# Kernel tuning notes

Measured on AMD Instinct MI355X. Metric: run time of the kernel, lower is better.

Reference implementation:

```python
import jax, jax.numpy as jnp
import numpy as np

B, H, C, PX, PY = 2, 16, 4, 16, 16
EXTRA = 64
HD = 64
N = C * PX * PY + EXTRA


def setup_inputs() -> dict:
    key = jax.random.key(0)
    ks = jax.random.split(key, 8)
    q = jax.random.normal(ks[0], (B, H, N, HD), jnp.float32)
    k = jax.random.normal(ks[1], (B, H, N, HD), jnp.float32)
    v = jax.random.normal(ks[2], (B, H, N, HD), jnp.float32)
    # valid SE(3) world-to-camera matrices: rotation via QR (det fixed to +1)
    A = jax.random.normal(ks[3], (B, C, 3, 3), jnp.float32)
    Q, _ = jnp.linalg.qr(A)
    det = jnp.linalg.det(Q)
    Q = Q * det[..., None, None]
    t = 0.5 * jax.random.normal(ks[4], (B, C, 3), jnp.float32)
    top = jnp.concatenate([Q, t[..., None]], -1)
    bot = jnp.broadcast_to(jnp.array([0.0, 0.0, 0.0, 1.0], jnp.float32), (B, C, 1, 4))
    viewmats = jnp.concatenate([top, bot], -2)
    # pinhole intrinsics (no skew)
    fx = 300.0 + 10.0 * jax.random.uniform(ks[5], (B, C))
    fy = 300.0 + 10.0 * jax.random.uniform(ks[6], (B, C))
    z = jnp.zeros((B, C)); o = jnp.ones((B, C))
    cx = 128.0 * o; cy = 128.0 * o
    Ks = jnp.stack([jnp.stack([fx, z, cx], -1), jnp.stack([z, fy, cy], -1), jnp.stack([z, z, o], -1)], -2)
    spatial_mask = jnp.arange(N) >= EXTRA  # first EXTRA tokens are non-spatial
    return {"q": q, "k": k, "v": v, "viewmats": viewmats, "Ks": Ks,
            "spatial_mask": spatial_mask, "patches_x": PX, "patches_y": PY,
            "image_width": 256, "image_height": 256}


def _invert_SE3(T):
    R = T[..., :3, :3]; t = T[..., :3, 3]
    Rinv = jnp.swapaxes(R, -1, -2)
    tinv = -jnp.einsum('...ij,...j->...i', Rinv, t)
    top = jnp.concatenate([Rinv, tinv[..., None]], -1)
    bot = jnp.broadcast_to(jnp.array([0.0, 0.0, 0.0, 1.0], T.dtype), T.shape[:-2] + (1, 4))
    return jnp.concatenate([top, bot], -2)


def _lift(K3):
    out = jnp.zeros(K3.shape[:-2] + (4, 4), K3.dtype)
    return out.at[..., :3, :3].set(K3).at[..., 3, 3].set(1.0)


def _invert_K(K):
    fx = K[..., 0, 0]; fy = K[..., 1, 1]; cx = K[..., 0, 2]; cy = K[..., 1, 2]
    z = jnp.zeros_like(fx); o = jnp.ones_like(fx)
    return jnp.stack([jnp.stack([1.0 / fx, z, -cx / fx], -1),
                      jnp.stack([z, 1.0 / fy, -cy / fy], -1),
                      jnp.stack([z, z, o], -1)], -2)


def _transform(feats, M, cosx, sinx, cosy, siny, inverse):
    # Block-diagonal: [tiled 4x4 projmat on D/2 | RoPE-x on D/4 | RoPE-y on D/4]
    Bq, Hq, Nq, D = feats.shape
    h2 = D // 2; h4 = D // 4
    p = feats[..., :h2].reshape(Bq, Hq, Nq, h2 // 4, 4)
    p = jnp.einsum('bnij,bhnkj->bhnki', M, p).reshape(Bq, Hq, Nq, h2)

    def rope(x, c, s):
        c = c[None, None]; s = s[None, None]  # [1,1,N,nf]
        xa, xb = x[..., : x.shape[-1] // 2], x[..., x.shape[-1] // 2:]
        if inverse:
            return jnp.concatenate([c * xa - s * xb, s * xa + c * xb], -1)
        return jnp.concatenate([c * xa + s * xb, -s * xa + c * xb], -1)

    rx = rope(feats[..., h2:h2 + h4], cosx, sinx)
    ry = rope(feats[..., h2 + h4:], cosy, siny)
    return jnp.concatenate([p, rx, ry], -1)


def reference(q, k, v, viewmats, Ks, spatial_mask, patches_x, patches_y, image_width, image_height):
    D = q.shape[-1]
    Bq, Cq = viewmats.shape[:2]
    # normalized intrinsics
    fx = Ks[..., 0, 0] / image_width; fy = Ks[..., 1, 1] / image_height
    cx = Ks[..., 0, 2] / image_width - 0.5; cy = Ks[..., 1, 2] / image_height - 0.5
    z = jnp.zeros_like(fx); o = jnp.ones_like(fx)
    Kn = jnp.stack([jnp.stack([fx, z, cx], -1), jnp.stack([z, fy, cy], -1), jnp.stack([z, z, o], -1)], -2)
    P = jnp.einsum('...ij,...jk->...ik', _lift(Kn), viewmats)          # [B,C,4,4]
    P_T = jnp.swapaxes(P, -1, -2)
    P_inv = jnp.einsum('...ij,...jk->...ik', _invert_SE3(viewmats), _lift(_invert_K(Kn)))
    # RoPE tables over spatial tokens (split convention, base=100, scale=1)
    nf = D // 8
    freqs = 100.0 ** (-jnp.arange(nf, dtype=jnp.float32) / nf)
    pos_x = jnp.tile(jnp.arange(patches_x, dtype=jnp.float32), patches_y * Cq)
    pos_y = jnp.tile(jnp.repeat(jnp.arange(patches_y, dtype=jnp.float32), patches_x), Cq)
    ang_x = pos_x[:, None] * freqs; ang_y = pos_y[:, None] * freqs  # [S,nf]
    mask = spatial_mask
    S = pos_x.shape[0]
    # index of each token within the spatial-token ordering (masked scatter, vectorized)
    sidx = jnp.clip(jnp.cumsum(mask.astype(jnp.int32)) - 1, 0, S - 1)
    m = mask[:, None]
    cosx = jnp.where(m, jnp.cos(ang_x)[sidx], 1.0); sinx = jnp.where(m, jnp.sin(ang_x)[sidx], 0.0)
    cosy = jnp.where(m, jnp.cos(ang_y)[sidx], 1.0); siny = jnp.where(m, jnp.sin(ang_y)[sidx], 0.0)
    cam = sidx // (patches_x * patches_y)  # camera id per token
    I4 = jnp.eye(4, dtype=q.dtype)
    mm = mask[None, :, None, None]
    Mq = jnp.where(mm, P_T[:, cam], I4)    # [B,N,4,4]
    Mkv = jnp.where(mm, P_inv[:, cam], I4)
    Mo = jnp.where(mm, P[:, cam], I4)
    qt = _transform(q, Mq, cosx, sinx, cosy, siny, False)
    kt = _transform(k, Mkv, cosx, sinx, cosy, siny, False)
    vt = _transform(v, Mkv, cosx, sinx, cosy, siny, False)
    logits = jnp.einsum('bhqd,bhkd->bhqk', qt, kt) / jnp.sqrt(jnp.float32(D))
    attn = jax.nn.softmax(logits, axis=-1)
    out = jnp.einsum('bhqk,bhkd->bhqd', attn, vt)
    return _transform(out, Mo, cosx, sinx, cosy, siny, True)
```

## Files before the change

### kernel.cpp

```cpp
#include <hip/hip_runtime.h>
#include <math.h>

typedef _Float16 f16;
typedef _Float16 f16x8 __attribute__((ext_vector_type(8)));
typedef __fp16 h16x2 __attribute__((ext_vector_type(2)));
typedef float f32x16 __attribute__((ext_vector_type(16)));
typedef unsigned int u32;
typedef u32 u32x4 __attribute__((ext_vector_type(4)));

constexpr int Bc = 2, Hc = 16, Cc = 4, PXc = 16, PYc = 16, EXTRAc = 64, HDc = 64;
constexpr int Nc = Cc * PXc * PYc + EXTRAc;
constexpr int BH = Bc * Hc;
constexpr int NKT = Nc / 64;
constexpr int NQT = Nc / 32;
constexpr int NBLK_F = NQT * BH;

constexpr size_t TENS_SZ  = (size_t)BH * Nc * HDc * 2;
constexpr size_t PBH      = (size_t)Nc * 128;
constexpr size_t QF_OFF   = 0;
constexpr size_t KF_OFF   = QF_OFF + TENS_SZ;
constexpr size_t VT_OFF   = KF_OFF + TENS_SZ;

__device__ const float FREQS[8] = {1.0f, 0.5623413252f, 0.31622776601f, 0.17782794100f,
                                   0.1f, 0.05623413252f, 0.031622776602f, 0.017782794100f};
constexpr float QSCALE = 0.125f * 1.4426950408889634f;

__device__ __forceinline__ void compute_M(float* M, const float* __restrict__ vm,
                                          const float* __restrict__ Ks3, int b, int cam, int which) {
    const float* V  = vm + (b * Cc + cam) * 16;
    const float* K3 = Ks3 + (b * Cc + cam) * 9;
    float fx = K3[0] * (1.0f / 256.0f);
    float fy = K3[4] * (1.0f / 256.0f);
    float cx = K3[2] * (1.0f / 256.0f) - 0.5f;
    float cy = K3[5] * (1.0f / 256.0f) - 0.5f;
    if (which == 2) {
        float IV[16];
        IV[0] = V[0]; IV[1] = V[4]; IV[2] = V[8];
        IV[4] = V[1]; IV[5] = V[5]; IV[6] = V[9];
        IV[8] = V[2]; IV[9] = V[6]; IV[10] = V[10];
        float tx = V[3], ty = V[7], tz = V[11];
        IV[3]  = -(IV[0] * tx + IV[1] * ty + IV[2] * tz);
        IV[7]  = -(IV[4] * tx + IV[5] * ty + IV[6] * tz);
        IV[11] = -(IV[8] * tx + IV[9] * ty + IV[10] * tz);
        IV[12] = 0.f; IV[13] = 0.f; IV[14] = 0.f; IV[15] = 1.f;
        float ifx = 1.f / fx, ify = 1.f / fy;
        float ncx = -cx * ifx, ncy = -cy * ify;
        #pragma unroll
        for (int i = 0; i < 4; ++i) {
            M[i * 4 + 0] = IV[i * 4 + 0] * ifx;
            M[i * 4 + 1] = IV[i * 4 + 1] * ify;
            M[i * 4 + 2] = IV[i * 4 + 0] * ncx + IV[i * 4 + 1] * ncy + IV[i * 4 + 2];
            M[i * 4 + 3] = IV[i * 4 + 3];
        }
    } else {
        float P[16];
        #pragma unroll
        for (int j = 0; j < 4; ++j) {
            P[0 * 4 + j] = fx * V[0 * 4 + j] + cx * V[2 * 4 + j];
            P[1 * 4 + j] = fy * V[1 * 4 + j] + cy * V[2 * 4 + j];
            P[2 * 4 + j] = V[2 * 4 + j];
            P[3 * 4 + j] = V[3 * 4 + j];
        }
        if (which == 0) {
            #pragma unroll
            for (int i = 0; i < 16; ++i) M[i] = P[i];
        } else {
            #pragma unroll
            for (int i = 0; i < 4; ++i)
                #pragma unroll
                for (int j = 0; j < 4; ++j) M[i * 4 + j] = P[j * 4 + i];
        }
    }
}

__device__ __forceinline__ void xf_seg_f(float* v16, int seg, int n, int b, int which,
                                         const float* __restrict__ vm, const float* __restrict__ Ks3,
                                         const float2 (*__restrict__ trig)[8]) {
    if (n < EXTRAc) return;
    int sidx = n - EXTRAc;
    int cam = sidx >> 8;
    if (seg < 2) {
        float M[16];
        compute_M(M, vm, Ks3, b, cam, which);
        #pragma unroll
        for (int g = 0; g < 4; ++g) {
            float a0 = v16[4 * g], a1 = v16[4 * g + 1], a2 = v16[4 * g + 2], a3 = v16[4 * g + 3];
            v16[4 * g + 0] = M[0]  * a0 + M[1]  * a1 + M[2]  * a2 + M[3]  * a3;
            v16[4 * g + 1] = M[4]  * a0 + M[5]  * a1 + M[6]  * a2 + M[7]  * a3;
            v16[4 * g + 2] = M[8]  * a0 + M[9]  * a1 + M[10] * a2 + M[11] * a3;
            v16[4 * g + 3] = M[12] * a0 + M[13] * a1 + M[14] * a2 + M[15] * a3;
        }
    } else {
        int pos = (seg == 2) ? (sidx & (PXc - 1)) : ((sidx >> 4) & (PYc - 1));
        #pragma unroll
        for (int f = 0; f < 8; ++f) {
            float2 cs = trig[pos][f];
            float xa = v16[f], xb = v16[8 + f];
            v16[f]     = cs.x * xa + cs.y * xb;
            v16[8 + f] = -cs.y * xa + cs.x * xb;
        }
    }
}

__device__ __forceinline__ u32 pkh(float a, float b) {
    h16x2 r = __builtin_amdgcn_cvt_pkrtz(a, b);
    return __builtin_bit_cast(u32, r);
}

__device__ __forceinline__ f32x16 zero16() {
    f32x16 z = {0.f,0.f,0.f,0.f,0.f,0.f,0.f,0.f,0.f,0.f,0.f,0.f,0.f,0.f,0.f,0.f};
    return z;
}

__global__ void prope_xform_kernel(const float* __restrict__ q, const float* __restrict__ k,
                                   const float* __restrict__ v,
                                   const float* __restrict__ viewmats, const float* __restrict__ Ks,
                                   char* __restrict__ wsb) {
    __shared__ f16 tile[64][72];
    __shared__ float2 trig[16][8];
    {
        int t = threadIdx.x;
        if (t < 128) {
            int p = t >> 3, f = t & 7;
            float s, c;
            __sincosf((float)p * FREQS[f], &s, &c);
            trig[p][f] = make_float2(c, s);
        }
    }
    __syncthreads();

    if (blockIdx.x < 1088) {
        int id = blockIdx.x * 256 + threadIdx.x;
        int seg = id & 3;
        int rid = id >> 2;
        int tensor = rid / (BH * Nc);
        int row = rid - tensor * (BH * Nc);
        int n = row % Nc;
        int bhq = row / Nc;
        int b = bhq >> 4;
        const float* src = (tensor ? k : q) + (size_t)row * 64 + seg * 16;
        float vals[16];
        #pragma unroll
        for (int i = 0; i < 4; ++i) ((float4*)vals)[i] = ((const float4*)src)[i];
        xf_seg_f(vals, seg, n, b, tensor ? 2 : 1, viewmats, Ks, trig);
        float scale = tensor ? 1.0f : QSCALE;
        f16 o[16];
        #pragma unroll
        for (int i = 0; i < 16; ++i) o[i] = (f16)(vals[i] * scale);
        if (tensor == 0) {
            char* base = wsb + QF_OFF + (size_t)bhq * PBH + (size_t)(n >> 5) * 4096;
            int qq = n & 31;
            *(float4*)(base + (seg * 2 + 0) * 512 + qq * 16) = ((float4*)o)[0];
            *(float4*)(base + (seg * 2 + 1) * 512 + qq * 16) = ((float4*)o)[1];
        } else {
            char* base = wsb + KF_OFF + (size_t)bhq * PBH + (size_t)(n >> 6) * 8192;
            int kk = n & 63, rh = kk >> 5, qq = kk & 31;
            *(float4*)(base + (((seg * 2 + rh) * 2 + 0) * 32 + qq) * 16) = ((float4*)o)[0];
            *(float4*)(base + (((seg * 2 + rh) * 2 + 1) * 32 + qq) * 16) = ((float4*)o)[1];
        }
    } else {
        int vb = blockIdx.x - 1088;
        int kt = vb >> 5, bh = vb & 31;
        int b = bh >> 4;
        int t = threadIdx.x;
        {
            int r = t >> 2, seg = t & 3;
            int n = kt * 64 + r;
            const float* src = v + ((size_t)bh * Nc + n) * 64 + seg * 16;
            float vals[16];
            #pragma unroll
            for (int i = 0; i < 4; ++i) ((float4*)vals)[i] = ((const float4*)src)[i];
            xf_seg_f(vals, seg, n, b, 2, viewmats, Ks, trig);
            #pragma unroll
            for (int i = 0; i < 16; ++i) tile[r][seg * 16 + i] = (f16)vals[i];
        }
        __syncthreads();
        {
            int d = t >> 2, ks = t & 3;
            f16 o[16];
            #pragma unroll
            for (int j = 0; j < 16; ++j) o[j] = tile[ks * 16 + j][d];
            int dh = d >> 5, dq = d & 31;
            char* base = wsb + VT_OFF + (size_t)bh * PBH + (size_t)kt * 8192;
            *(float4*)(base + (((ks * 2 + dh) * 2 + 0) * 32 + dq) * 16) = ((float4*)o)[0];
            *(float4*)(base + (((ks * 2 + dh) * 2 + 1) * 32 + dq) * 16) = ((float4*)o)[1];
        }
    }
}

__global__ __launch_bounds__(256, 4) void prope_attn_fused_kernel(
    const char* __restrict__ wsb, const float* __restrict__ viewmats,
    const float* __restrict__ Ks, float* __restrict__ out) {
    __shared__ float os[4][32][64];
    __shared__ float mls[4][32];

    const int tid = threadIdx.x;
    const int wv = tid >> 6, lane = tid & 63;
    const int q = lane & 31, h = lane >> 5;
    const int bid = blockIdx.x;
    const int l = (bid & 7) * (NBLK_F / 8) + (bid >> 3);
    const int qt = l % NQT;
    const int bh = l / NQT;
    const int ts = (NKT * wv) / 4, te = (NKT * (wv + 1)) / 4;

    const char* kfb = wsb + KF_OFF + (size_t)bh * PBH;
    const char* vfb = wsb + VT_OFF + (size_t)bh * PBH;
    const char* qfb = wsb + QF_OFF + (size_t)bh * PBH + (size_t)qt * 4096;

    f16x8 qb[4];
    #pragma unroll
    for (int c = 0; c < 4; ++c) qb[c] = *(const f16x8*)(qfb + c * 1024 + lane * 16);

    const f32x16 M8 = {-8.f,-8.f,-8.f,-8.f,-8.f,-8.f,-8.f,-8.f,
                       -8.f,-8.f,-8.f,-8.f,-8.f,-8.f,-8.f,-8.f};

    f32x16 o0 = zero16(), o1 = zero16();
    float lloc = 0.f;

    for (int it = ts; it < te; ++it) {
        const char* kb = kfb + (size_t)it * 8192;
        const char* vb = vfb + (size_t)it * 8192;
        f16x8 ka0[4], ka1[4];
        #pragma unroll
        for (int c = 0; c < 4; ++c) {
            ka0[c] = *(const f16x8*)(kb + (c * 2 + 0) * 1024 + lane * 16);
            ka1[c] = *(const f16x8*)(kb + (c * 2 + 1) * 1024 + lane * 16);
        }
        f32x16 s0 = M8, s1 = M8;
        #pragma unroll
        for (int c = 0; c < 4; ++c) {
            s0 = __builtin_amdgcn_mfma_f32_32x32x16_f16(ka0[c], qb[c], s0, 0, 0, 0);
            s1 = __builtin_amdgcn_mfma_f32_32x32x16_f16(ka1[c], qb[c], s1, 0, 0, 0);
        }
        f16x8 va0[4], va1[4];
        #pragma unroll
        for (int c = 0; c < 4; ++c) {
            va0[c] = *(const f16x8*)(vb + (c * 2 + 0) * 1024 + lane * 16);
            va1[c] = *(const f16x8*)(vb + (c * 2 + 1) * 1024 + lane * 16);
        }
        #pragma unroll
        for (int i = 0; i < 16; ++i) s0[i] = exp2f(s0[i]);
        #pragma unroll
        for (int i = 0; i < 16; ++i) s1[i] = exp2f(s1[i]);
        float a8[8];
        #pragma unroll
        for (int i = 0; i < 4; ++i) {
            a8[i]     = (s0[4*i] + s0[4*i+1]) + (s0[4*i+2] + s0[4*i+3]);
            a8[4 + i] = (s1[4*i] + s1[4*i+1]) + (s1[4*i+2] + s1[4*i+3]);
        }
        lloc += ((a8[0] + a8[1]) + (a8[2] + a8[3])) + ((a8[4] + a8[5]) + (a8[6] + a8[7]));

        u32 U0[8], U1[8];
        #pragma unroll
        for (int g = 0; g < 4; ++g) {
            U0[g * 2 + 0] = pkh(s0[4 * g + 0], s0[4 * g + 1]);
            U0[g * 2 + 1] = pkh(s0[4 * g + 2], s0[4 * g + 3]);
            U1[g * 2 + 0] = pkh(s1[4 * g + 0], s1[4 * g + 1]);
            U1[g * 2 + 1] = pkh(s1[4 * g + 2], s1[4 * g + 3]);
        }
        u32 pw[4][4];
        #pragma unroll
        for (int c = 0; c < 4; ++c) {
            const u32* Us = (c < 2) ? U0 : U1;
            int gl = 2 * (c & 1);
            u32 x0 = Us[(gl + 1) * 2 + 0], x1 = Us[(gl + 1) * 2 + 1];
            u32 y0 = Us[gl * 2 + 0],       y1 = Us[gl * 2 + 1];
            u32 s0w = h ? y0 : x0;
            u32 s1w = h ? y1 : x1;
            u32 r0 = (u32)__shfl_xor((int)s0w, 32, 64);
            u32 r1 = (u32)__shfl_xor((int)s1w, 32, 64);
            u32 own0 = h ? x0 : y0, own1 = h ? x1 : y1;
            pw[c][0] = h ? r0 : own0;
            pw[c][1] = h ? r1 : own1;
            pw[c][2] = h ? own0 : r0;
            pw[c][3] = h ? own1 : r1;
        }
        #pragma unroll
        for (int c = 0; c < 4; ++c) {
            u32x4 fw = {pw[c][0], pw[c][1], pw[c][2], pw[c][3]};
            f16x8 pb = __builtin_bit_cast(f16x8, fw);
            o0 = __builtin_amdgcn_mfma_f32_32x32x16_f16(va0[c], pb, o0, 0, 0, 0);
            o1 = __builtin_amdgcn_mfma_f32_32x32x16_f16(va1[c], pb, o1, 0, 0, 0);
        }
    }

    #pragma unroll
    for (int i = 0; i < 16; ++i) {
        os[wv][i][lane]      = o0[i];
        os[wv][16 + i][lane] = o1[i];
    }
    {
        float lw = lloc + __shfl_xor(lloc, 32, 64);
        if (h == 0) mls[wv][q] = lw;
    }
    __syncthreads();

    float linv = 1.f / (mls[0][q] + mls[1][q] + mls[2][q] + mls[3][q]);
    float acc[8];
    #pragma unroll
    for (int j = 0; j < 8; ++j) {
        int i = 8 * wv + j;
        acc[j] = (os[0][i][lane] + os[1][i][lane] + os[2][i][lane] + os[3][i][lane]) * linv;
    }

    const int n = qt * 32 + q;
    if (qt >= 2) {
        int sidx = n - EXTRAc;
        int cam = sidx >> 8, b = bh >> 4;
        if (wv < 2) {
            float M[16];
            compute_M(M, viewmats, Ks, b, cam, 0);
            #pragma unroll
            for (int g2 = 0; g2 < 2; ++g2) {
                float a0 = acc[4*g2], a1 = acc[4*g2+1], a2 = acc[4*g2+2], a3 = acc[4*g2+3];
                acc[4*g2+0] = M[0]  * a0 + M[1]  * a1 + M[2]  * a2 + M[3]  * a3;
                acc[4*g2+1] = M[4]  * a0 + M[5]  * a1 + M[6]  * a2 + M[7]  * a3;
                acc[4*g2+2] = M[8]  * a0 + M[9]  * a1 + M[10] * a2 + M[11] * a3;
                acc[4*g2+3] = M[12] * a0 + M[13] * a1 + M[14] * a2 + M[15] * a3;
            }
        } else {
            float pos = (wv == 2) ? (float)(sidx & (PXc - 1)) : (float)((sidx >> 4) & (PYc - 1));
            #pragma unroll
            for (int j = 0; j < 4; ++j) {
                float s, c;
                __sincosf(pos * FREQS[j + 4 * h], &s, &c);
                float xa = acc[j], xb = acc[4 + j];
                acc[j]     = c * xa - s * xb;
                acc[4 + j] = s * xa + c * xb;
            }
        }
    }

    float* go = out + ((size_t)bh * Nc + n) * 64 + 16 * wv + 4 * h;
    float4 v0 = {acc[0], acc[1], acc[2], acc[3]};
    float4 v1 = {acc[4], acc[5], acc[6], acc[7]};
    *(float4*)go = v0;
    *(float4*)(go + 8) = v1;
}

extern "C" void kernel_launch(void* const* d_in, const int* in_sizes, int n_in,
                              void* d_out, int out_size, void* d_ws, size_t ws_size,
                              hipStream_t stream) {
    const float* q        = (const float*)d_in[0];
    const float* k        = (const float*)d_in[1];
    const float* v        = (const float*)d_in[2];
    const float* viewmats = (const float*)d_in[3];
    const float* Ks       = (const float*)d_in[4];
    char* wsb  = (char*)d_ws;
    float* out = (float*)d_out;

    prope_xform_kernel<<<1088 + 544, 256, 0, stream>>>(q, k, v, viewmats, Ks, wsb);
    prope_attn_fused_kernel<<<NBLK_F, 256, 0, stream>>>(wsb, viewmats, Ks, out);
}
```

Measured before the change: 46.53 us.

## Merge transform and attention kernels into one cooperative persistent kernel

Replaces the two launches (transform and attention) with a single cooperative kernel. Blocks grid-stride over the transform work items, then synchronise with a grid barrier, then grid-stride over the attention tiles, with shared memory reused between the two phases. The intent is to remove the second launch and the gap between kernels. In exchange it adds a grid-wide barrier, an occupancy query on the host each call, and lower occupancy than the earlier launch-bounds hint, and the grid is capped at the number of attention tiles.

```diff
diff --git a/kernel.cpp b/kernel.cpp
--- a/kernel.cpp
+++ b/kernel.cpp
@@ -1,5 +1,8 @@
 #include <hip/hip_runtime.h>
+#include <hip/hip_cooperative_groups.h>
 #include <math.h>
+
+namespace cg = cooperative_groups;
 
 typedef _Float16 f16;
 typedef _Float16 f16x8 __attribute__((ext_vector_type(8)));
@@ -14,6 +17,7 @@
 constexpr int NKT = Nc / 64;
 constexpr int NQT = Nc / 32;
 constexpr int NBLK_F = NQT * BH;
+constexpr int NXF = 1632;
 
 constexpr size_t TENS_SZ  = (size_t)BH * Nc * HDc * 2;
 constexpr size_t PBH      = (size_t)Nc * 128;
@@ -112,230 +116,233 @@
     return z;
 }
 
-__global__ void prope_xform_kernel(const float* __restrict__ q, const float* __restrict__ k,
-                                   const float* __restrict__ v,
-                                   const float* __restrict__ viewmats, const float* __restrict__ Ks,
-                                   char* __restrict__ wsb) {
-    __shared__ f16 tile[64][72];
-    __shared__ float2 trig[16][8];
+__global__ __launch_bounds__(256) void prope_fused_all(
+    const float* __restrict__ q, const float* __restrict__ k, const float* __restrict__ v,
+    const float* __restrict__ viewmats, const float* __restrict__ Ks,
+    char* __restrict__ wsb, float* __restrict__ out)
+{
+    __shared__ __align__(16) char sbuf[33280];
+    const int tid = threadIdx.x;
+
     {
-        int t = threadIdx.x;
-        if (t < 128) {
-            int p = t >> 3, f = t & 7;
+        auto trig = reinterpret_cast<float2(*)[8]>(sbuf);
+        auto tile = reinterpret_cast<f16(*)[72]>(sbuf + 1024);
+        if (tid < 128) {
+            int p = tid >> 3, f = tid & 7;
             float s, c;
             __sincosf((float)p * FREQS[f], &s, &c);
             trig[p][f] = make_float2(c, s);
         }
+        for (int item = blockIdx.x; item < NXF; item += gridDim.x) {
+            __syncthreads();
+            if (item < 1088) {
+                int id = item * 256 + tid;
+                int seg = id & 3;
+                int rid = id >> 2;
+                int tensor = rid / (BH * Nc);
+                int row = rid - tensor * (BH * Nc);
+                int n = row % Nc;
+                int bhq = row / Nc;
+                int b = bhq >> 4;
+                const float* src = (tensor ? k : q) + (size_t)row * 64 + seg * 16;
+                float vals[16];
+                #pragma unroll
+                for (int i = 0; i < 4; ++i) ((float4*)vals)[i] = ((const float4*)src)[i];
+                xf_seg_f(vals, seg, n, b, tensor ? 2 : 1, viewmats, Ks, trig);
+                float scale = tensor ? 1.0f : QSCALE;
+                f16 o[16];
+                #pragma unroll
+                for (int i = 0; i < 16; ++i) o[i] = (f16)(vals[i] * scale);
+                if (tensor == 0) {
+                    char* base = wsb + QF_OFF + (size_t)bhq * PBH + (size_t)(n >> 5) * 4096;
+                    int qq = n & 31;
+                    *(float4*)(base + (seg * 2 + 0) * 512 + qq * 16) = ((float4*)o)[0];
+                    *(float4*)(base + (seg * 2 + 1) * 512 + qq * 16) = ((float4*)o)[1];
+                } else {
+                    char* base = wsb + KF_OFF + (size_t)bhq * PBH + (size_t)(n >> 6) * 8192;
+                    int kk = n & 63, rh = kk >> 5, qq = kk & 31;
+                    *(float4*)(base + (((seg * 2 + rh) * 2 + 0) * 32 + qq) * 16) = ((float4*)o)[0];
+                    *(float4*)(base + (((seg * 2 + rh) * 2 + 1) * 32 + qq) * 16) = ((float4*)o)[1];
+                }
+            } else {
+                int vbi = item - 1088;
+                int kt = vbi >> 5, bh = vbi & 31;
+                int b = bh >> 4;
+                {
+                    int r = tid >> 2, seg = tid & 3;
+                    int n = kt * 64 + r;
+                    const float* src = v + ((size_t)bh * Nc + n) * 64 + seg * 16;
+                    float vals[16];
+                    #pragma unroll
+                    for (int i = 0; i < 4; ++i) ((float4*)vals)[i] = ((const float4*)src)[i];
+                    xf_seg_f(vals, seg, n, b, 2, viewmats, Ks, trig);
+                    #pragma unroll
+                    for (int i = 0; i < 16; ++i) tile[r][seg * 16 + i] = (f16)vals[i];
+                }
+                __syncthreads();
+                {
+                    int d = tid >> 2, ks = tid & 3;
+                    f16 o[16];
+                    #pragma unroll
+                    for (int j = 0; j < 16; ++j) o[j] = tile[ks * 16 + j][d];
+                    int dh = d >> 5, dq = d & 31;
+                    char* base = wsb + VT_OFF + (size_t)bh * PBH + (size_t)kt * 8192;
+                    *(float4*)(base + (((ks * 2 + dh) * 2 + 0) * 32 + dq) * 16) = ((float4*)o)[0];
+                    *(float4*)(base + (((ks * 2 + dh) * 2 + 1) * 32 + dq) * 16) = ((float4*)o)[1];
+                }
+            }
+        }
     }
-    __syncthreads();
-
-    if (blockIdx.x < 1088) {
-        int id = blockIdx.x * 256 + threadIdx.x;
-        int seg = id & 3;
-        int rid = id >> 2;
-        int tensor = rid / (BH * Nc);
-        int row = rid - tensor * (BH * Nc);
-        int n = row % Nc;
-        int bhq = row / Nc;
-        int b = bhq >> 4;
-        const float* src = (tensor ? k : q) + (size_t)row * 64 + seg * 16;
-        float vals[16];
-        #pragma unroll
-        for (int i = 0; i < 4; ++i) ((float4*)vals)[i] = ((const float4*)src)[i];
-        xf_seg_f(vals, seg, n, b, tensor ? 2 : 1, viewmats, Ks, trig);
-        float scale = tensor ? 1.0f : QSCALE;
-        f16 o[16];
-        #pragma unroll
-        for (int i = 0; i < 16; ++i) o[i] = (f16)(vals[i] * scale);
-        if (tensor == 0) {
-            char* base = wsb + QF_OFF + (size_t)bhq * PBH + (size_t)(n >> 5) * 4096;
-            int qq = n & 31;
-            *(float4*)(base + (seg * 2 + 0) * 512 + qq * 16) = ((float4*)o)[0];
-            *(float4*)(base + (seg * 2 + 1) * 512 + qq * 16) = ((float4*)o)[1];
-        } else {
-            char* base = wsb + KF_OFF + (size_t)bhq * PBH + (size_t)(n >> 6) * 8192;
-            int kk = n & 63, rh = kk >> 5, qq = kk & 31;
-            *(float4*)(base + (((seg * 2 + rh) * 2 + 0) * 32 + qq) * 16) = ((float4*)o)[0];
-            *(float4*)(base + (((seg * 2 + rh) * 2 + 1) * 32 + qq) * 16) = ((float4*)o)[1];
-        }
-    } else {
-        int vb = blockIdx.x - 1088;
-        int kt = vb >> 5, bh = vb & 31;
-        int b = bh >> 4;
-        int t = threadIdx.x;
-        {
-            int r = t >> 2, seg = t & 3;
-            int n = kt * 64 + r;
-            const float* src = v + ((size_t)bh * Nc + n) * 64 + seg * 16;
-            float vals[16];
-            #pragma unroll
-            for (int i = 0; i < 4; ++i) ((float4*)vals)[i] = ((const float4*)src)[i];
-            xf_seg_f(vals, seg, n, b, 2, viewmats, Ks, trig);
-            #pragma unroll
-            for (int i = 0; i < 16; ++i) tile[r][seg * 16 + i] = (f16)vals[i];
-        }
-        __syncthreads();
-        {
-            int d = t >> 2, ks = t & 3;
-            f16 o[16];
-            #pragma unroll
-            for (int j = 0; j < 16; ++j) o[j] = tile[ks * 16 + j][d];
-            int dh = d >> 5, dq = d & 31;
-            char* base = wsb + VT_OFF + (size_t)bh * PBH + (size_t)kt * 8192;
-            *(float4*)(base + (((ks * 2 + dh) * 2 + 0) * 32 + dq) * 16) = ((float4*)o)[0];
-            *(float4*)(base + (((ks * 2 + dh) * 2 + 1) * 32 + dq) * 16) = ((float4*)o)[1];
-        }
-    }
-}
-
-__global__ __launch_bounds__(256, 4) void prope_attn_fused_kernel(
-    const char* __restrict__ wsb, const float* __restrict__ viewmats,
-    const float* __restrict__ Ks, float* __restrict__ out) {
-    __shared__ float os[4][32][64];
-    __shared__ float mls[4][32];
-
-    const int tid = threadIdx.x;
+
+    __threadfence();
+    cg::this_grid().sync();
+
+    auto os  = reinterpret_cast<float(*)[32][64]>(sbuf);
+    auto mls = reinterpret_cast<float(*)[32]>(sbuf + 32768);
     const int wv = tid >> 6, lane = tid & 63;
-    const int q = lane & 31, h = lane >> 5;
-    const int bid = blockIdx.x;
-    const int l = (bid & 7) * (NBLK_F / 8) + (bid >> 3);
-    const int qt = l % NQT;
-    const int bh = l / NQT;
+    const int ql = lane & 31, h = lane >> 5;
     const int ts = (NKT * wv) / 4, te = (NKT * (wv + 1)) / 4;
-
-    const char* kfb = wsb + KF_OFF + (size_t)bh * PBH;
-    const char* vfb = wsb + VT_OFF + (size_t)bh * PBH;
-    const char* qfb = wsb + QF_OFF + (size_t)bh * PBH + (size_t)qt * 4096;
-
-    f16x8 qb[4];
-    #pragma unroll
-    for (int c = 0; c < 4; ++c) qb[c] = *(const f16x8*)(qfb + c * 1024 + lane * 16);
 
     const f32x16 M8 = {-8.f,-8.f,-8.f,-8.f,-8.f,-8.f,-8.f,-8.f,
                        -8.f,-8.f,-8.f,-8.f,-8.f,-8.f,-8.f,-8.f};
 
-    f32x16 o0 = zero16(), o1 = zero16();
-    float lloc = 0.f;
-
-    for (int it = ts; it < te; ++it) {
-        const char* kb = kfb + (size_t)it * 8192;
-        const char* vb = vfb + (size_t)it * 8192;
-        f16x8 ka0[4], ka1[4];
-        #pragma unroll
-        for (int c = 0; c < 4; ++c) {
-            ka0[c] = *(const f16x8*)(kb + (c * 2 + 0) * 1024 + lane * 16);
-            ka1[c] = *(const f16x8*)(kb + (c * 2 + 1) * 1024 + lane * 16);
-        }
-        f32x16 s0 = M8, s1 = M8;
-        #pragma unroll
-        for (int c = 0; c < 4; ++c) {
-            s0 = __builtin_amdgcn_mfma_f32_32x32x16_f16(ka0[c], qb[c], s0, 0, 0, 0);
-            s1 = __builtin_amdgcn_mfma_f32_32x32x16_f16(ka1[c], qb[c], s1, 0, 0, 0);
-        }
-        f16x8 va0[4], va1[4];
-        #pragma unroll
-        for (int c = 0; c < 4; ++c) {
-            va0[c] = *(const f16x8*)(vb + (c * 2 + 0) * 1024 + lane * 16);
-            va1[c] = *(const f16x8*)(vb + (c * 2 + 1) * 1024 + lane * 16);
-        }
-        #pragma unroll
-        for (int i = 0; i < 16; ++i) s0[i] = exp2f(s0[i]);
-        #pragma unroll
-        for (int i = 0; i < 16; ++i) s1[i] = exp2f(s1[i]);
-        float a8[8];
-        #pragma unroll
-        for (int i = 0; i < 4; ++i) {
-            a8[i]     = (s0[4*i] + s0[4*i+1]) + (s0[4*i+2] + s0[4*i+3]);
-            a8[4 + i] = (s1[4*i] + s1[4*i+1]) + (s1[4*i+2] + s1[4*i+3]);
-        }
-        lloc += ((a8[0] + a8[1]) + (a8[2] + a8[3])) + ((a8[4] + a8[5]) + (a8[6] + a8[7]));
-
-        u32 U0[8], U1[8];
-        #pragma unroll
-        for (int g = 0; g < 4; ++g) {
-            U0[g * 2 + 0] = pkh(s0[4 * g + 0], s0[4 * g + 1]);
-            U0[g * 2 + 1] = pkh(s0[4 * g + 2], s0[4 * g + 3]);
-            U1[g * 2 + 0] = pkh(s1[4 * g + 0], s1[4 * g + 1]);
-            U1[g * 2 + 1] = pkh(s1[4 * g + 2], s1[4 * g + 3]);
-        }
-        u32 pw[4][4];
-        #pragma unroll
-        for (int c = 0; c < 4; ++c) {
-            const u32* Us = (c < 2) ? U0 : U1;
-            int gl = 2 * (c & 1);
-            u32 x0 = Us[(gl + 1) * 2 + 0], x1 = Us[(gl + 1) * 2 + 1];
-            u32 y0 = Us[gl * 2 + 0],       y1 = Us[gl * 2 + 1];
-            u32 s0w = h ? y0 : x0;
-            u32 s1w = h ? y1 : x1;
-            u32 r0 = (u32)__shfl_xor((int)s0w, 32, 64);
-            u32 r1 = (u32)__shfl_xor((int)s1w, 32, 64);
-            u32 own0 = h ? x0 : y0, own1 = h ? x1 : y1;
-            pw[c][0] = h ? r0 : own0;
-            pw[c][1] = h ? r1 : own1;
-            pw[c][2] = h ? own0 : r0;
-            pw[c][3] = h ? own1 : r1;
-        }
-        #pragma unroll
-        for (int c = 0; c < 4; ++c) {
-            u32x4 fw = {pw[c][0], pw[c][1], pw[c][2], pw[c][3]};
-            f16x8 pb = __builtin_bit_cast(f16x8, fw);
-            o0 = __builtin_amdgcn_mfma_f32_32x32x16_f16(va0[c], pb, o0, 0, 0, 0);
-            o1 = __builtin_amdgcn_mfma_f32_32x32x16_f16(va1[c], pb, o1, 0, 0, 0);
-        }
+    for (int item = blockIdx.x; item < NBLK_F; item += gridDim.x) {
+        __syncthreads();
+        const int l = (item & 7) * (NBLK_F / 8) + (item >> 3);
+        const int qt = l % NQT;
+        const int bh = l / NQT;
+
+        const char* kfb = wsb + KF_OFF + (size_t)bh * PBH;
+        const char* vfb = wsb + VT_OFF + (size_t)bh * PBH;
+        const char* qfb = wsb + QF_OFF + (size_t)bh * PBH + (size_t)qt * 4096;
+
+        f16x8 qb[4];
+        #pragma unroll
+        for (int c = 0; c < 4; ++c) qb[c] = *(const f16x8*)(qfb + c * 1024 + lane * 16);
+
+        f32x16 o0 = zero16(), o1 = zero16();
+        float lloc = 0.f;
+
+        for (int it = ts; it < te; ++it) {
+            const char* kb = kfb + (size_t)it * 8192;
+            const char* vb = vfb + (size_t)it * 8192;
+            f16x8 ka0[4], ka1[4];
+            #pragma unroll
+            for (int c = 0; c < 4; ++c) {
+                ka0[c] = *(const f16x8*)(kb + (c * 2 + 0) * 1024 + lane * 16);
+                ka1[c] = *(const f16x8*)(kb + (c * 2 + 1) * 1024 + lane * 16);
+            }
+            f32x16 s0 = M8, s1 = M8;
+            #pragma unroll
+            for (int c = 0; c < 4; ++c) {
+                s0 = __builtin_amdgcn_mfma_f32_32x32x16_f16(ka0[c], qb[c], s0, 0, 0, 0);
+                s1 = __builtin_amdgcn_mfma_f32_32x32x16_f16(ka1[c], qb[c], s1, 0, 0, 0);
+            }
+            f16x8 va0[4], va1[4];
+            #pragma unroll
+            for (int c = 0; c < 4; ++c) {
+                va0[c] = *(const f16x8*)(vb + (c * 2 + 0) * 1024 + lane * 16);
+                va1[c] = *(const f16x8*)(vb + (c * 2 + 1) * 1024 + lane * 16);
+            }
+            #pragma unroll
+            for (int i = 0; i < 16; ++i) s0[i] = exp2f(s0[i]);
+            #pragma unroll
+            for (int i = 0; i < 16; ++i) s1[i] = exp2f(s1[i]);
+            float a8[8];
+            #pragma unroll
+            for (int i = 0; i < 4; ++i) {
+                a8[i]     = (s0[4*i] + s0[4*i+1]) + (s0[4*i+2] + s0[4*i+3]);
+                a8[4 + i] = (s1[4*i] + s1[4*i+1]) + (s1[4*i+2] + s1[4*i+3]);
+            }
+            lloc += ((a8[0] + a8[1]) + (a8[2] + a8[3])) + ((a8[4] + a8[5]) + (a8[6] + a8[7]));
+
+            u32 U0[8], U1[8];
+            #pragma unroll
+            for (int g = 0; g < 4; ++g) {
+                U0[g * 2 + 0] = pkh(s0[4 * g + 0], s0[4 * g + 1]);
+                U0[g * 2 + 1] = pkh(s0[4 * g + 2], s0[4 * g + 3]);
+                U1[g * 2 + 0] = pkh(s1[4 * g + 0], s1[4 * g + 1]);
+                U1[g * 2 + 1] = pkh(s1[4 * g + 2], s1[4 * g + 3]);
+            }
+            u32 pw[4][4];
+            #pragma unroll
+            for (int c = 0; c < 4; ++c) {
+                const u32* Us = (c < 2) ? U0 : U1;
+                int gl = 2 * (c & 1);
+                u32 x0 = Us[(gl + 1) * 2 + 0], x1 = Us[(gl + 1) * 2 + 1];
+                u32 y0 = Us[gl * 2 + 0],       y1 = Us[gl * 2 + 1];
+                u32 s0w = h ? y0 : x0;
+                u32 s1w = h ? y1 : x1;
+                u32 r0 = (u32)__shfl_xor((int)s0w, 32, 64);
+                u32 r1 = (u32)__shfl_xor((int)s1w, 32, 64);
+                u32 own0 = h ? x0 : y0, own1 = h ? x1 : y1;
+                pw[c][0] = h ? r0 : own0;
+                pw[c][1] = h ? r1 : own1;
+                pw[c][2] = h ? own0 : r0;
+                pw[c][3] = h ? own1 : r1;
+            }
+            #pragma unroll
+            for (int c = 0; c < 4; ++c) {
+                u32x4 fw = {pw[c][0], pw[c][1], pw[c][2], pw[c][3]};
+                f16x8 pb = __builtin_bit_cast(f16x8, fw);
+                o0 = __builtin_amdgcn_mfma_f32_32x32x16_f16(va0[c], pb, o0, 0, 0, 0);
+                o1 = __builtin_amdgcn_mfma_f32_32x32x16_f16(va1[c], pb, o1, 0, 0, 0);
+            }
+        }
+
+        #pragma unroll
+        for (int i = 0; i < 16; ++i) {
+            os[wv][i][lane]      = o0[i];
+            os[wv][16 + i][lane] = o1[i];
+        }
+        {
+            float lw = lloc + __shfl_xor(lloc, 32, 64);
+            if (h == 0) mls[wv][ql] = lw;
+        }
+        __syncthreads();
+
+        float linv = 1.f / (mls[0][ql] + mls[1][ql] + mls[2][ql] + mls[3][ql]);
+        float acc[8];
+        #pragma unroll
+        for (int j = 0; j < 8; ++j) {
+            int i = 8 * wv + j;
+            acc[j] = (os[0][i][lane] + os[1][i][lane] + os[2][i][lane] + os[3][i][lane]) * linv;
+        }
+
+        const int n = qt * 32 + ql;
+        if (qt >= 2) {
+            int sidx = n - EXTRAc;
+            int cam = sidx >> 8, b = bh >> 4;
+            if (wv < 2) {
+                float M[16];
+                compute_M(M, viewmats, Ks, b, cam, 0);
+                #pragma unroll
+                for (int g2 = 0; g2 < 2; ++g2) {
+                    float a0 = acc[4*g2], a1 = acc[4*g2+1], a2 = acc[4*g2+2], a3 = acc[4*g2+3];
+                    acc[4*g2+0] = M[0]  * a0 + M[1]  * a1 + M[2]  * a2 + M[3]  * a3;
+                    acc[4*g2+1] = M[4]  * a0 + M[5]  * a1 + M[6]  * a2 + M[7]  * a3;
+                    acc[4*g2+2] = M[8]  * a0 + M[9]  * a1 + M[10] * a2 + M[11] * a3;
+                    acc[4*g2+3] = M[12] * a0 + M[13] * a1 + M[14] * a2 + M[15] * a3;
+                }
+            } else {
+                float pos = (wv == 2) ? (float)(sidx & (PXc - 1)) : (float)((sidx >> 4) & (PYc - 1));
+                #pragma unroll
+                for (int j = 0; j < 4; ++j) {
+                    float s, c;
+                    __sincosf(pos * FREQS[j + 4 * h], &s, &c);
+                    float xa = acc[j], xb = acc[4 + j];
+                    acc[j]     = c * xa - s * xb;
+                    acc[4 + j] = s * xa + c * xb;
+                }
+            }
+        }
+
+        float* go = out + ((size_t)bh * Nc + n) * 64 + 16 * wv + 4 * h;
+        float4 v0 = {acc[0], acc[1], acc[2], acc[3]};
+        float4 v1 = {acc[4], acc[5], acc[6], acc[7]};
+        *(float4*)go = v0;
+        *(float4*)(go + 8) = v1;
     }
-
-    #pragma unroll
-    for (int i = 0; i < 16; ++i) {
-        os[wv][i][lane]      = o0[i];
-        os[wv][16 + i][lane] = o1[i];
-    }
-    {
-        float lw = lloc + __shfl_xor(lloc, 32, 64);
-        if (h == 0) mls[wv][q] = lw;
-    }
-    __syncthreads();
-
-    float linv = 1.f / (mls[0][q] + mls[1][q] + mls[2][q] + mls[3][q]);
-    float acc[8];
-    #pragma unroll
-    for (int j = 0; j < 8; ++j) {
-        int i = 8 * wv + j;
-        acc[j] = (os[0][i][lane] + os[1][i][lane] + os[2][i][lane] + os[3][i][lane]) * linv;
-    }
-
-    const int n = qt * 32 + q;
-    if (qt >= 2) {
-        int sidx = n - EXTRAc;
-        int cam = sidx >> 8, b = bh >> 4;
-        if (wv < 2) {
-            float M[16];
-            compute_M(M, viewmats, Ks, b, cam, 0);
-            #pragma unroll
-            for (int g2 = 0; g2 < 2; ++g2) {
-                float a0 = acc[4*g2], a1 = acc[4*g2+1], a2 = acc[4*g2+2], a3 = acc[4*g2+3];
-                acc[4*g2+0] = M[0]  * a0 + M[1]  * a1 + M[2]  * a2 + M[3]  * a3;
-                acc[4*g2+1] = M[4]  * a0 + M[5]  * a1 + M[6]  * a2 + M[7]  * a3;
-                acc[4*g2+2] = M[8]  * a0 + M[9]  * a1 + M[10] * a2 + M[11] * a3;
-                acc[4*g2+3] = M[12] * a0 + M[13] * a1 + M[14] * a2 + M[15] * a3;
-            }
-        } else {
-            float pos = (wv == 2) ? (float)(sidx & (PXc - 1)) : (float)((sidx >> 4) & (PYc - 1));
-            #pragma unroll
-            for (int j = 0; j < 4; ++j) {
-                float s, c;
-                __sincosf(pos * FREQS[j + 4 * h], &s, &c);
-                float xa = acc[j], xb = acc[4 + j];
-                acc[j]     = c * xa - s * xb;
-                acc[4 + j] = s * xa + c * xb;
-            }
-        }
-    }
-
-    float* go = out + ((size_t)bh * Nc + n) * 64 + 16 * wv + 4 * h;
-    float4 v0 = {acc[0], acc[1], acc[2], acc[3]};
-    float4 v1 = {acc[4], acc[5], acc[6], acc[7]};
-    *(float4*)go = v0;
-    *(float4*)(go + 8) = v1;
 }
 
 extern "C" void kernel_launch(void* const* d_in, const int* in_sizes, int n_in,
@@ -349,6 +356,13 @@
     char* wsb  = (char*)d_ws;
     float* out = (float*)d_out;
 
-    prope_xform_kernel<<<1088 + 544, 256, 0, stream>>>(q, k, v, viewmats, Ks, wsb);
-    prope_attn_fused_kernel<<<NBLK_F, 256, 0, stream>>>(wsb, viewmats, Ks, out);
-}
+    int nb = 0;
+    hipOccupancyMaxActiveBlocksPerMultiprocessor(&nb, prope_fused_all, 256, 0);
+    if (nb < 1) nb = 1;
+    unsigned int grid = (unsigned int)nb * 256u;
+    if (grid > (unsigned int)NBLK_F) grid = NBLK_F;
+
+    void* args[] = {(void*)&q, (void*)&k, (void*)&v, (void*)&viewmats, (void*)&Ks,
+                    (void*)&wsb, (void*)&out};
+    hipLaunchCooperativeKernel(prope_fused_all, dim3(grid), dim3(256), args, 0, stream);
+}
```

After: 120.5 us. +158.9%, slower.
